# Optimization experiments

Measured on AMD Instinct MI355X. Metric: run time of the kernel, lower is better.

## Reference

```python
import jax, jax.numpy as jnp
import numpy as np

E = 1024  # embed_dim
H = 16    # num_heads
D = E // H  # head_dim


def setup_inputs() -> dict:
    key = jax.random.key(0)
    ks = jax.random.split(key, 9)
    s = 0.02
    return {
        "hidden_state": jax.random.normal(ks[0], (4, 1024, E), jnp.float32),
        "Wq": jax.random.normal(ks[1], (H, D, E), jnp.float32) * s,
        "bq": jax.random.normal(ks[2], (H, D), jnp.float32) * s,
        "Wk": jax.random.normal(ks[3], (H, D, E), jnp.float32) * s,
        "bk": jax.random.normal(ks[4], (H, D), jnp.float32) * s,
        "Wv": jax.random.normal(ks[5], (H, D, E), jnp.float32) * s,
        "bv": jax.random.normal(ks[6], (H, D), jnp.float32) * s,
        "Wo": jax.random.normal(ks[7], (E, E), jnp.float32) * s,
        "bo": jax.random.normal(ks[8], (E,), jnp.float32) * s,
    }


def _mha(x, Wq, bq, Wk, bk, Wv, bv, Wo, bo):
    # Per-head linear projections (torch Linear: y = x W^T + b), batched over heads.
    q = jnp.einsum("bse,hde->bhsd", x, Wq) + bq[None, :, None, :]
    k = jnp.einsum("bse,hde->bhsd", x, Wk) + bk[None, :, None, :]
    v = jnp.einsum("bse,hde->bhsd", x, Wv) + bv[None, :, None, :]
    scores = jnp.einsum("bhsd,bhtd->bhst", q, k) / jnp.sqrt(jnp.asarray(D, x.dtype))
    w = jax.nn.softmax(scores, axis=-1)  # F.softmax default -> last dim
    o = jnp.einsum("bhst,bhtd->bhsd", w, v)
    # concat heads along last dim: [B,S,H*D] in head order (matches torch.cat)
    B, _, S, _ = o.shape
    o = jnp.transpose(o, (0, 2, 1, 3)).reshape(B, S, H * D)
    return o @ Wo.T + bo


def reference(hidden_state, Wq, bq, Wk, bk, Wv, bv, Wo, bo):
    return _mha(hidden_state, Wq, bq, Wk, bk, Wv, bv, Wo, bo)
```

## Files before the change

kernel.cpp:

```cpp
#include <hip/hip_runtime.h>
#include <hip/hip_bf16.h>
#include <stdint.h>

#define E_DIM 1024
#define H_NUM 16
#define D_DIM 64
#define B_NUM 4
#define S_LEN 1024

typedef __attribute__((ext_vector_type(8))) short bf16x8;
typedef __attribute__((ext_vector_type(4))) short bf16x4;
typedef __attribute__((ext_vector_type(4))) float f32x4;

#define SOFTMAX_C2 0.18033688011112042f

__device__ inline ushort f2b(float x) {
    __hip_bfloat16 h = __float2bfloat16(x);
    return *(ushort*)&h;
}
__device__ inline uint pk2(float a, float b) {
    __hip_bfloat162 h = __float22bfloat162_rn(make_float2(a, b));
    return *(uint*)&h;
}

__device__ inline void gld16(const ushort* g, ushort* l) {
    __builtin_amdgcn_global_load_lds((const __attribute__((address_space(1))) void*)g,
                                     (__attribute__((address_space(3))) void*)l, 16, 0, 0);
}

__global__ __launch_bounds__(256)
void convert_all(const float* __restrict__ X,  const float* __restrict__ Wq,
                 const float* __restrict__ Wk, const float* __restrict__ Wv,
                 const float* __restrict__ Wo,
                 ushort* __restrict__ Xb, ushort* __restrict__ Wcat,
                 ushort* __restrict__ Wob)
{
    const int bid = blockIdx.x;
    const float* src; ushort* dst; size_t off;
    if (bid < 4096)      { src = X;  dst = Xb;   off = (size_t)bid * 1024; }
    else if (bid < 5120) { src = Wq; dst = Wcat;              off = (size_t)(bid - 4096) * 1024; }
    else if (bid < 6144) { src = Wk; dst = Wcat + (1u << 20); off = (size_t)(bid - 5120) * 1024; }
    else if (bid < 7168) { src = Wv; dst = Wcat + (2u << 20); off = (size_t)(bid - 6144) * 1024; }
    else                 { src = Wo; dst = Wob;               off = (size_t)(bid - 7168) * 1024; }
    const size_t i = off + (size_t)threadIdx.x * 4;
    float4 v = *(const float4*)&src[i];
    ushort4 o;
    o.x = f2b(v.x); o.y = f2b(v.y); o.z = f2b(v.z); o.w = f2b(v.w);
    *(ushort4*)&dst[i] = o;
}

template<int MODE>
__global__ __launch_bounds__(256)
void gemm128(const ushort* __restrict__ A, const ushort* __restrict__ Bw,
             const float* __restrict__ b0, const float* __restrict__ b1,
             const float* __restrict__ b2,
             ushort* __restrict__ Qb, ushort* __restrict__ Kb,
             ushort* __restrict__ Vt_g, float* __restrict__ Cout, int K)
{
    __shared__ __align__(16) ushort SM[12288];
    ushort* As = SM;
    ushort* Bs = SM + 8192;

    const int tid  = threadIdx.x;
    const int wave = tid >> 6;
    const int lane = tid & 63;
    const int quad = lane >> 4;
    const int l16  = lane & 15;
    const int wm   = wave & 1;
    const int wn   = wave >> 1;
    const int m0   = blockIdx.x * 128;
    const int n0   = blockIdx.y * 64;

    f32x4 acc[4][2] = {};

#pragma unroll
    for (int i = 0; i < 2; ++i) {
        const int e = i * 256 + tid;
        gld16(&A[(size_t)(m0 + (e >> 2)) * K + (e & 3) * 8], &As[e * 8]);
    }
    gld16(&Bw[(size_t)(n0 + (tid >> 2)) * K + (tid & 3) * 8], &Bs[tid * 8]);
    __syncthreads();

    const int nk = K >> 5;
    for (int ki = 0; ki < nk; ++ki) {
        const int cur = ki & 1;
        if (ki + 1 < nk) {
            const int k0 = (ki + 1) << 5;
#pragma unroll
            for (int i = 0; i < 2; ++i) {
                const int e = i * 256 + tid;
                gld16(&A[(size_t)(m0 + (e >> 2)) * K + k0 + (e & 3) * 8],
                      &As[(cur ^ 1) * 4096 + e * 8]);
            }
            gld16(&Bw[(size_t)(n0 + (tid >> 2)) * K + k0 + (tid & 3) * 8],
                  &Bs[(cur ^ 1) * 2048 + tid * 8]);
        }

        bf16x8 af[4], bf[2];
#pragma unroll
        for (int mi = 0; mi < 4; ++mi)
            af[mi] = *(const bf16x8*)&As[cur * 4096 + (wm * 64 + mi * 16 + l16) * 32 + quad * 8];
#pragma unroll
        for (int ni = 0; ni < 2; ++ni)
            bf[ni] = *(const bf16x8*)&Bs[cur * 2048 + (wn * 32 + ni * 16 + l16) * 32 + quad * 8];
#pragma unroll
        for (int mi = 0; mi < 4; ++mi)
#pragma unroll
            for (int ni = 0; ni < 2; ++ni)
                acc[mi][ni] = __builtin_amdgcn_mfma_f32_16x16x32_bf16(af[mi], bf[ni], acc[mi][ni], 0, 0, 0);
        __syncthreads();
    }

    if (MODE == 0) {
        const int seg   = n0 >> 10;
        const int cbase = n0 & 1023;
        const float* bp = (seg == 0) ? b0 : (seg == 1) ? b1 : b2;
        const float scl = (seg == 0) ? SOFTMAX_C2 : 1.0f;

        if (seg < 2) {
            ushort* T = SM;
#pragma unroll
            for (int ni = 0; ni < 2; ++ni) {
                const int nloc = wn * 32 + ni * 16 + l16;
                const float bv = bp[cbase + nloc];
#pragma unroll
                for (int mi = 0; mi < 4; ++mi)
#pragma unroll
                    for (int r = 0; r < 4; ++r)
                        T[(wm * 64 + mi * 16 + quad * 4 + r) * 72 + nloc] =
                            f2b((acc[mi][ni][r] + bv) * scl);
            }
            __syncthreads();
            ushort* dst = (seg == 0) ? Qb : Kb;
            const int row = tid >> 1, half = tid & 1;
            const ushort* s = &T[row * 72 + half * 32];
            ushort* d = &dst[(size_t)(m0 + row) * 1024 + cbase + half * 32];
#pragma unroll
            for (int j = 0; j < 4; ++j)
                *(uint4*)(d + j * 8) = *(const uint4*)(s + j * 8);
        } else {
            ushort* Tt = SM;
            const int hh = cbase >> 6;
            const int b  = m0 >> 10, sbase = m0 & 1023;
#pragma unroll
            for (int ni = 0; ni < 2; ++ni) {
                const int nloc = wn * 32 + ni * 16 + l16;
                const float bv = bp[cbase + nloc];
#pragma unroll
                for (int mi = 0; mi < 4; ++mi) {
                    const int mloc = wm * 64 + mi * 16 + quad * 4;
                    ushort4 pk;
                    pk.x = f2b(acc[mi][ni][0] + bv);
                    pk.y = f2b(acc[mi][ni][1] + bv);
                    pk.z = f2b(acc[mi][ni][2] + bv);
                    pk.w = f2b(acc[mi][ni][3] + bv);
                    *(ushort4*)&Tt[nloc * 136 + mloc] = pk;
                }
            }
            __syncthreads();
            const int nrow = tid >> 2, qtr = tid & 3;
            const ushort* s = &Tt[nrow * 136 + qtr * 32];
            ushort* d = &Vt_g[(((size_t)(b * 16 + hh)) * 64 + nrow) * 1024 + sbase + qtr * 32];
#pragma unroll
            for (int j = 0; j < 4; ++j)
                *(uint4*)(d + j * 8) = *(const uint4*)(s + j * 8);
        }
    } else {
        float* Tf = (float*)SM;
        float bv[2];
#pragma unroll
        for (int ni = 0; ni < 2; ++ni)
            bv[ni] = b0[n0 + wn * 32 + ni * 16 + l16];
#pragma unroll
        for (int p = 0; p < 2; ++p) {
            if (wm == p) {
#pragma unroll
                for (int ni = 0; ni < 2; ++ni) {
                    const int nloc = wn * 32 + ni * 16 + l16;
#pragma unroll
                    for (int mi = 0; mi < 4; ++mi)
#pragma unroll
                        for (int r = 0; r < 4; ++r)
                            Tf[(mi * 16 + quad * 4 + r) * 68 + nloc] = acc[mi][ni][r] + bv[ni];
                }
            }
            __syncthreads();
            const int row = tid >> 2, q4 = tid & 3;
            const float* s = &Tf[row * 68 + q4 * 16];
            float* d = &Cout[(size_t)(m0 + p * 64 + row) * 1024 + n0 + q4 * 16];
#pragma unroll
            for (int j = 0; j < 4; ++j)
                *(float4*)(d + j * 4) = *(const float4*)(s + j * 4);
            __syncthreads();
        }
    }
}

__global__ __launch_bounds__(256)
void attention5(const ushort* __restrict__ Qg, const ushort* __restrict__ Kg,
                const ushort* __restrict__ Vg, ushort* __restrict__ Og)
{
    __shared__ ushort S[4][64][68];

    const int tid  = threadIdx.x;
    const int w    = tid >> 6;
    const int lane = tid & 63;
    const int quad = lane >> 4;
    const int l16  = lane & 15;

    const int qt = blockIdx.x;
    const int bh = blockIdx.y;
    const int b  = bh >> 4;
    const int h  = bh & 15;
    const size_t tbase = ((size_t)b * S_LEN) * E_DIM + (size_t)h * D_DIM;
    const size_t vbase = (size_t)bh * D_DIM * S_LEN;

    const int sr = tid >> 3;
    const int c8 = (tid & 7) * 8;

#pragma unroll
    for (int g = 0; g < 4; ++g) {
        const int rr = sr + g * 32;
        *(uint4*)&S[2 + (rr >> 6)][rr & 63][c8] =
            *(const uint4*)&Qg[tbase + (size_t)(qt * 128 + rr) * E_DIM + c8];
    }
#pragma unroll
    for (int g = 0; g < 2; ++g) {
        const int rr = sr + g * 32;
        *(uint4*)&S[0][rr][c8] = *(const uint4*)&Kg[tbase + (size_t)rr * E_DIM + c8];
        *(uint4*)&S[1][rr][c8] = *(const uint4*)&Vg[vbase + (size_t)rr * S_LEN + c8];
    }
    __syncthreads();

    bf16x8 qf[2][2];
#pragma unroll
    for (int u = 0; u < 2; ++u) {
        qf[u][0] = *(const bf16x8*)&S[2 + u][w * 16 + l16][quad * 8];
        qf[u][1] = *(const bf16x8*)&S[2 + u][w * 16 + l16][32 + quad * 8];
    }
    __syncthreads();

    float lq[2] = {0.0f, 0.0f};
    f32x4 oacc[2][4] = {};

    for (int kt = 0; kt < 16; ++kt) {
        const int cur = kt & 1;

        uint4 kpre[2], vpre[2];
        if (kt < 15) {
#pragma unroll
            for (int g = 0; g < 2; ++g) {
                const int rr = sr + g * 32;
                kpre[g] = *(const uint4*)&Kg[tbase + (size_t)((kt + 1) * 64 + rr) * E_DIM + c8];
                vpre[g] = *(const uint4*)&Vg[vbase + (size_t)rr * S_LEN + (kt + 1) * 64 + c8];
            }
        }

        f32x4 sacc[2][4] = {};
#pragma unroll
        for (int mt = 0; mt < 4; ++mt)
#pragma unroll
            for (int ks = 0; ks < 2; ++ks) {
                bf16x8 kf = *(const bf16x8*)&S[cur * 2][mt * 16 + l16][ks * 32 + quad * 8];
                sacc[0][mt] = __builtin_amdgcn_mfma_f32_16x16x32_bf16(kf, qf[0][ks], sacc[0][mt], 0, 0, 0);
                sacc[1][mt] = __builtin_amdgcn_mfma_f32_16x16x32_bf16(kf, qf[1][ks], sacc[1][mt], 0, 0, 0);
            }

        bf16x4 pf[2][4];
#pragma unroll
        for (int u = 0; u < 2; ++u) {
            float rs = 0.0f;
#pragma unroll
            for (int mt = 0; mt < 4; ++mt) {
                float p0 = exp2f(sacc[u][mt][0]);
                float p1 = exp2f(sacc[u][mt][1]);
                float p2 = exp2f(sacc[u][mt][2]);
                float p3 = exp2f(sacc[u][mt][3]);
                rs += (p0 + p1) + (p2 + p3);
                union { uint uu[2]; bf16x4 v; } pk;
                pk.uu[0] = pk2(p0, p1);
                pk.uu[1] = pk2(p2, p3);
                pf[u][mt] = pk.v;
            }
            lq[u] += rs;
        }

#pragma unroll
        for (int nb = 0; nb < 4; ++nb)
#pragma unroll
            for (int kb = 0; kb < 4; ++kb) {
                bf16x4 vf = *(const bf16x4*)&S[cur * 2 + 1][nb * 16 + l16][kb * 16 + quad * 4];
                oacc[0][nb] = __builtin_amdgcn_mfma_f32_16x16x16bf16_1k(pf[0][kb], vf, oacc[0][nb], 0, 0, 0);
                oacc[1][nb] = __builtin_amdgcn_mfma_f32_16x16x16bf16_1k(pf[1][kb], vf, oacc[1][nb], 0, 0, 0);
            }

        if (kt < 15) {
            const int nxt = cur ^ 1;
#pragma unroll
            for (int g = 0; g < 2; ++g) {
                const int rr = sr + g * 32;
                *(uint4*)&S[nxt * 2][rr][c8]     = kpre[g];
                *(uint4*)&S[nxt * 2 + 1][rr][c8] = vpre[g];
            }
        }
        __syncthreads();
    }

#pragma unroll
    for (int u = 0; u < 2; ++u) {
        float l = lq[u];
        l += __shfl_xor(l, 16);
        l += __shfl_xor(l, 32);
        const float linv = 1.0f / l;
        float lC[4];
#pragma unroll
        for (int r = 0; r < 4; ++r) lC[r] = __shfl(linv, quad * 4 + r);
#pragma unroll
        for (int nb = 0; nb < 4; ++nb)
#pragma unroll
            for (int r = 0; r < 4; ++r) {
                const int q = qt * 128 + u * 64 + w * 16 + quad * 4 + r;
                const int d = nb * 16 + l16;
                Og[tbase + (size_t)q * E_DIM + d] = f2b(oacc[u][nb][r] * lC[r]);
            }
    }
}

extern "C" void kernel_launch(void* const* d_in, const int* in_sizes, int n_in,
                              void* d_out, int out_size, void* d_ws, size_t ws_size,
                              hipStream_t stream)
{
    (void)in_sizes; (void)n_in; (void)out_size; (void)ws_size;

    const float* X  = (const float*)d_in[0];
    const float* Wq = (const float*)d_in[1];
    const float* bq = (const float*)d_in[2];
    const float* Wk = (const float*)d_in[3];
    const float* bk = (const float*)d_in[4];
    const float* Wv = (const float*)d_in[5];
    const float* bv = (const float*)d_in[6];
    const float* Wo = (const float*)d_in[7];
    const float* bo = (const float*)d_in[8];

    const size_t MEG = 1u << 20;
    ushort* ws   = (ushort*)d_ws;
    ushort* Xb   = ws;
    ushort* Wcat = ws + 4 * MEG;
    ushort* Wob  = ws + 7 * MEG;
    ushort* Qb   = ws + 8 * MEG;
    ushort* Kb   = ws + 12 * MEG;
    ushort* Vtg  = ws + 16 * MEG;
    ushort* AO   = Xb;

    dim3 blk(256);

    convert_all<<<8192, blk, 0, stream>>>(X, Wq, Wk, Wv, Wo, Xb, Wcat, Wob);

    gemm128<0><<<dim3(32, 48), blk, 0, stream>>>(Xb, Wcat, bq, bk, bv,
                                                 Qb, Kb, Vtg, nullptr, E_DIM);

    attention5<<<dim3(8, 64), blk, 0, stream>>>(Qb, Kb, Vtg, AO);

    gemm128<1><<<dim3(32, 16), blk, 0, stream>>>(AO, Wob, bo, nullptr, nullptr,
                                                 nullptr, nullptr, nullptr,
                                                 (float*)d_out, E_DIM);
}
```

Measured before the change: 208.1 us.

## Split attention over key halves with combine kernel and smaller output-GEMM tiles

Attention is now split along the key dimension into two halves (grid z=2) with 64-query tiles and 32-key steps. Each half writes unnormalised bf16 partial outputs and row sums, which a new combine kernel adds and normalises into the head-concatenated buffer. The output projection becomes a dedicated 64x64-tile GEMM to launch more blocks. This raises block count and occupancy on the many-CU GPU, at the cost of an extra kernel launch, extra partial-result traffic, and rounding partials to bf16 before summing.

```diff
diff --git a/kernel.cpp b/kernel.cpp
--- a/kernel.cpp
+++ b/kernel.cpp
@@ -17,6 +17,10 @@
 __device__ inline ushort f2b(float x) {
     __hip_bfloat16 h = __float2bfloat16(x);
     return *(ushort*)&h;
+}
+__device__ inline float b2f(ushort u) {
+    __hip_bfloat16 h = *(__hip_bfloat16*)&u;
+    return __bfloat162float(h);
 }
 __device__ inline uint pk2(float a, float b) {
     __hip_bfloat162 h = __float22bfloat162_rn(make_float2(a, b));
@@ -49,13 +53,12 @@
     *(ushort4*)&dst[i] = o;
 }
 
-template<int MODE>
 __global__ __launch_bounds__(256)
-void gemm128(const ushort* __restrict__ A, const ushort* __restrict__ Bw,
-             const float* __restrict__ b0, const float* __restrict__ b1,
-             const float* __restrict__ b2,
-             ushort* __restrict__ Qb, ushort* __restrict__ Kb,
-             ushort* __restrict__ Vt_g, float* __restrict__ Cout, int K)
+void gemm_qkv(const ushort* __restrict__ A, const ushort* __restrict__ Bw,
+              const float* __restrict__ b0, const float* __restrict__ b1,
+              const float* __restrict__ b2,
+              ushort* __restrict__ Qb, ushort* __restrict__ Kb,
+              ushort* __restrict__ Vt_g, int K)
 {
     __shared__ __align__(16) ushort SM[12288];
     ushort* As = SM;
@@ -111,96 +114,68 @@
         __syncthreads();
     }
 
-    if (MODE == 0) {
-        const int seg   = n0 >> 10;
-        const int cbase = n0 & 1023;
-        const float* bp = (seg == 0) ? b0 : (seg == 1) ? b1 : b2;
-        const float scl = (seg == 0) ? SOFTMAX_C2 : 1.0f;
-
-        if (seg < 2) {
-            ushort* T = SM;
-#pragma unroll
-            for (int ni = 0; ni < 2; ++ni) {
-                const int nloc = wn * 32 + ni * 16 + l16;
-                const float bv = bp[cbase + nloc];
-#pragma unroll
-                for (int mi = 0; mi < 4; ++mi)
-#pragma unroll
-                    for (int r = 0; r < 4; ++r)
-                        T[(wm * 64 + mi * 16 + quad * 4 + r) * 72 + nloc] =
-                            f2b((acc[mi][ni][r] + bv) * scl);
+    const int seg   = n0 >> 10;
+    const int cbase = n0 & 1023;
+    const float* bp = (seg == 0) ? b0 : (seg == 1) ? b1 : b2;
+    const float scl = (seg == 0) ? SOFTMAX_C2 : 1.0f;
+
+    if (seg < 2) {
+        ushort* T = SM;
+#pragma unroll
+        for (int ni = 0; ni < 2; ++ni) {
+            const int nloc = wn * 32 + ni * 16 + l16;
+            const float bv = bp[cbase + nloc];
+#pragma unroll
+            for (int mi = 0; mi < 4; ++mi)
+#pragma unroll
+                for (int r = 0; r < 4; ++r)
+                    T[(wm * 64 + mi * 16 + quad * 4 + r) * 72 + nloc] =
+                        f2b((acc[mi][ni][r] + bv) * scl);
+        }
+        __syncthreads();
+        ushort* dst = (seg == 0) ? Qb : Kb;
+        const int row = tid >> 1, half = tid & 1;
+        const ushort* s = &T[row * 72 + half * 32];
+        ushort* d = &dst[(size_t)(m0 + row) * 1024 + cbase + half * 32];
+#pragma unroll
+        for (int j = 0; j < 4; ++j)
+            *(uint4*)(d + j * 8) = *(const uint4*)(s + j * 8);
+    } else {
+        ushort* Tt = SM;
+        const int hh = cbase >> 6;
+        const int b  = m0 >> 10, sbase = m0 & 1023;
+#pragma unroll
+        for (int ni = 0; ni < 2; ++ni) {
+            const int nloc = wn * 32 + ni * 16 + l16;
+            const float bv = bp[cbase + nloc];
+#pragma unroll
+            for (int mi = 0; mi < 4; ++mi) {
+                const int mloc = wm * 64 + mi * 16 + quad * 4;
+                ushort4 pk;
+                pk.x = f2b(acc[mi][ni][0] + bv);
+                pk.y = f2b(acc[mi][ni][1] + bv);
+                pk.z = f2b(acc[mi][ni][2] + bv);
+                pk.w = f2b(acc[mi][ni][3] + bv);
+                *(ushort4*)&Tt[nloc * 136 + mloc] = pk;
             }
-            __syncthreads();
-            ushort* dst = (seg == 0) ? Qb : Kb;
-            const int row = tid >> 1, half = tid & 1;
-            const ushort* s = &T[row * 72 + half * 32];
-            ushort* d = &dst[(size_t)(m0 + row) * 1024 + cbase + half * 32];
-#pragma unroll
-            for (int j = 0; j < 4; ++j)
-                *(uint4*)(d + j * 8) = *(const uint4*)(s + j * 8);
-        } else {
-            ushort* Tt = SM;
-            const int hh = cbase >> 6;
-            const int b  = m0 >> 10, sbase = m0 & 1023;
-#pragma unroll
-            for (int ni = 0; ni < 2; ++ni) {
-                const int nloc = wn * 32 + ni * 16 + l16;
-                const float bv = bp[cbase + nloc];
-#pragma unroll
-                for (int mi = 0; mi < 4; ++mi) {
-                    const int mloc = wm * 64 + mi * 16 + quad * 4;
-                    ushort4 pk;
-                    pk.x = f2b(acc[mi][ni][0] + bv);
-                    pk.y = f2b(acc[mi][ni][1] + bv);
-                    pk.z = f2b(acc[mi][ni][2] + bv);
-                    pk.w = f2b(acc[mi][ni][3] + bv);
-                    *(ushort4*)&Tt[nloc * 136 + mloc] = pk;
-                }
-            }
-            __syncthreads();
-            const int nrow = tid >> 2, qtr = tid & 3;
-            const ushort* s = &Tt[nrow * 136 + qtr * 32];
-            ushort* d = &Vt_g[(((size_t)(b * 16 + hh)) * 64 + nrow) * 1024 + sbase + qtr * 32];
-#pragma unroll
-            for (int j = 0; j < 4; ++j)
-                *(uint4*)(d + j * 8) = *(const uint4*)(s + j * 8);
-        }
-    } else {
-        float* Tf = (float*)SM;
-        float bv[2];
-#pragma unroll
-        for (int ni = 0; ni < 2; ++ni)
-            bv[ni] = b0[n0 + wn * 32 + ni * 16 + l16];
-#pragma unroll
-        for (int p = 0; p < 2; ++p) {
-            if (wm == p) {
-#pragma unroll
-                for (int ni = 0; ni < 2; ++ni) {
-                    const int nloc = wn * 32 + ni * 16 + l16;
-#pragma unroll
-                    for (int mi = 0; mi < 4; ++mi)
-#pragma unroll
-                        for (int r = 0; r < 4; ++r)
-                            Tf[(mi * 16 + quad * 4 + r) * 68 + nloc] = acc[mi][ni][r] + bv[ni];
-                }
-            }
-            __syncthreads();
-            const int row = tid >> 2, q4 = tid & 3;
-            const float* s = &Tf[row * 68 + q4 * 16];
-            float* d = &Cout[(size_t)(m0 + p * 64 + row) * 1024 + n0 + q4 * 16];
-#pragma unroll
-            for (int j = 0; j < 4; ++j)
-                *(float4*)(d + j * 4) = *(const float4*)(s + j * 4);
-            __syncthreads();
-        }
+        }
+        __syncthreads();
+        const int nrow = tid >> 2, qtr = tid & 3;
+        const ushort* s = &Tt[nrow * 136 + qtr * 32];
+        ushort* d = &Vt_g[(((size_t)(b * 16 + hh)) * 64 + nrow) * 1024 + sbase + qtr * 32];
+#pragma unroll
+        for (int j = 0; j < 4; ++j)
+            *(uint4*)(d + j * 8) = *(const uint4*)(s + j * 8);
     }
 }
 
 __global__ __launch_bounds__(256)
-void attention5(const ushort* __restrict__ Qg, const ushort* __restrict__ Kg,
-                const ushort* __restrict__ Vg, ushort* __restrict__ Og)
-{
-    __shared__ ushort S[4][64][68];
+void attention6(const ushort* __restrict__ Qg, const ushort* __restrict__ Kg,
+                const ushort* __restrict__ Vg,
+                ushort* __restrict__ Opart, float* __restrict__ Lpart)
+{
+    __shared__ ushort Kb[2][32][72];
+    __shared__ ushort Vb[2][64][40];
 
     const int tid  = threadIdx.x;
     const int w    = tid >> 6;
@@ -210,119 +185,187 @@
 
     const int qt = blockIdx.x;
     const int bh = blockIdx.y;
+    const int th = blockIdx.z;
     const int b  = bh >> 4;
     const int h  = bh & 15;
     const size_t tbase = ((size_t)b * S_LEN) * E_DIM + (size_t)h * D_DIM;
     const size_t vbase = (size_t)bh * D_DIM * S_LEN;
-
-    const int sr = tid >> 3;
-    const int c8 = (tid & 7) * 8;
-
-#pragma unroll
-    for (int g = 0; g < 4; ++g) {
-        const int rr = sr + g * 32;
-        *(uint4*)&S[2 + (rr >> 6)][rr & 63][c8] =
-            *(const uint4*)&Qg[tbase + (size_t)(qt * 128 + rr) * E_DIM + c8];
-    }
-#pragma unroll
-    for (int g = 0; g < 2; ++g) {
-        const int rr = sr + g * 32;
-        *(uint4*)&S[0][rr][c8] = *(const uint4*)&Kg[tbase + (size_t)rr * E_DIM + c8];
-        *(uint4*)&S[1][rr][c8] = *(const uint4*)&Vg[vbase + (size_t)rr * S_LEN + c8];
+    const int t0 = th * 512;
+
+    const ushort* qrow = Qg + tbase + (size_t)(qt * 64 + w * 16 + l16) * E_DIM + quad * 8;
+    bf16x8 qf[2];
+    qf[0] = *(const bf16x8*)qrow;
+    qf[1] = *(const bf16x8*)(qrow + 32);
+
+    {
+        const int kr = tid >> 3, kc = (tid & 7) * 8;
+        *(uint4*)&Kb[0][kr][kc] = *(const uint4*)&Kg[tbase + (size_t)(t0 + kr) * E_DIM + kc];
+        const int vr = tid >> 2, vc = (tid & 3) * 8;
+        *(uint4*)&Vb[0][vr][vc] = *(const uint4*)&Vg[vbase + (size_t)vr * S_LEN + t0 + vc];
     }
     __syncthreads();
 
-    bf16x8 qf[2][2];
-#pragma unroll
-    for (int u = 0; u < 2; ++u) {
-        qf[u][0] = *(const bf16x8*)&S[2 + u][w * 16 + l16][quad * 8];
-        qf[u][1] = *(const bf16x8*)&S[2 + u][w * 16 + l16][32 + quad * 8];
-    }
-    __syncthreads();
-
-    float lq[2] = {0.0f, 0.0f};
-    f32x4 oacc[2][4] = {};
+    float lq = 0.0f;
+    f32x4 oacc[4] = {};
 
     for (int kt = 0; kt < 16; ++kt) {
         const int cur = kt & 1;
 
-        uint4 kpre[2], vpre[2];
+        uint4 kpre, vpre;
+        const int kr = tid >> 3, kc = (tid & 7) * 8;
+        const int vr = tid >> 2, vc = (tid & 3) * 8;
         if (kt < 15) {
-#pragma unroll
-            for (int g = 0; g < 2; ++g) {
-                const int rr = sr + g * 32;
-                kpre[g] = *(const uint4*)&Kg[tbase + (size_t)((kt + 1) * 64 + rr) * E_DIM + c8];
-                vpre[g] = *(const uint4*)&Vg[vbase + (size_t)rr * S_LEN + (kt + 1) * 64 + c8];
+            const int tg = t0 + (kt + 1) * 32;
+            kpre = *(const uint4*)&Kg[tbase + (size_t)(tg + kr) * E_DIM + kc];
+            vpre = *(const uint4*)&Vg[vbase + (size_t)vr * S_LEN + tg + vc];
+        }
+
+        f32x4 sacc[2] = {};
+#pragma unroll
+        for (int mt = 0; mt < 2; ++mt)
+#pragma unroll
+            for (int ks = 0; ks < 2; ++ks) {
+                bf16x8 kf = *(const bf16x8*)&Kb[cur][mt * 16 + l16][ks * 32 + quad * 8];
+                sacc[mt] = __builtin_amdgcn_mfma_f32_16x16x32_bf16(kf, qf[ks], sacc[mt], 0, 0, 0);
             }
-        }
-
-        f32x4 sacc[2][4] = {};
-#pragma unroll
-        for (int mt = 0; mt < 4; ++mt)
-#pragma unroll
-            for (int ks = 0; ks < 2; ++ks) {
-                bf16x8 kf = *(const bf16x8*)&S[cur * 2][mt * 16 + l16][ks * 32 + quad * 8];
-                sacc[0][mt] = __builtin_amdgcn_mfma_f32_16x16x32_bf16(kf, qf[0][ks], sacc[0][mt], 0, 0, 0);
-                sacc[1][mt] = __builtin_amdgcn_mfma_f32_16x16x32_bf16(kf, qf[1][ks], sacc[1][mt], 0, 0, 0);
-            }
-
-        bf16x4 pf[2][4];
-#pragma unroll
-        for (int u = 0; u < 2; ++u) {
-            float rs = 0.0f;
-#pragma unroll
-            for (int mt = 0; mt < 4; ++mt) {
-                float p0 = exp2f(sacc[u][mt][0]);
-                float p1 = exp2f(sacc[u][mt][1]);
-                float p2 = exp2f(sacc[u][mt][2]);
-                float p3 = exp2f(sacc[u][mt][3]);
-                rs += (p0 + p1) + (p2 + p3);
-                union { uint uu[2]; bf16x4 v; } pk;
-                pk.uu[0] = pk2(p0, p1);
-                pk.uu[1] = pk2(p2, p3);
-                pf[u][mt] = pk.v;
-            }
-            lq[u] += rs;
-        }
+
+        bf16x4 pf[2];
+        float rs = 0.0f;
+#pragma unroll
+        for (int mt = 0; mt < 2; ++mt) {
+            float p0 = exp2f(sacc[mt][0]);
+            float p1 = exp2f(sacc[mt][1]);
+            float p2 = exp2f(sacc[mt][2]);
+            float p3 = exp2f(sacc[mt][3]);
+            rs += (p0 + p1) + (p2 + p3);
+            union { uint uu[2]; bf16x4 v; } pk;
+            pk.uu[0] = pk2(p0, p1);
+            pk.uu[1] = pk2(p2, p3);
+            pf[mt] = pk.v;
+        }
+        lq += rs;
 
 #pragma unroll
         for (int nb = 0; nb < 4; ++nb)
 #pragma unroll
-            for (int kb = 0; kb < 4; ++kb) {
-                bf16x4 vf = *(const bf16x4*)&S[cur * 2 + 1][nb * 16 + l16][kb * 16 + quad * 4];
-                oacc[0][nb] = __builtin_amdgcn_mfma_f32_16x16x16bf16_1k(pf[0][kb], vf, oacc[0][nb], 0, 0, 0);
-                oacc[1][nb] = __builtin_amdgcn_mfma_f32_16x16x16bf16_1k(pf[1][kb], vf, oacc[1][nb], 0, 0, 0);
+            for (int kb = 0; kb < 2; ++kb) {
+                bf16x4 vf = *(const bf16x4*)&Vb[cur][nb * 16 + l16][kb * 16 + quad * 4];
+                oacc[nb] = __builtin_amdgcn_mfma_f32_16x16x16bf16_1k(pf[kb], vf, oacc[nb], 0, 0, 0);
             }
 
         if (kt < 15) {
             const int nxt = cur ^ 1;
-#pragma unroll
-            for (int g = 0; g < 2; ++g) {
-                const int rr = sr + g * 32;
-                *(uint4*)&S[nxt * 2][rr][c8]     = kpre[g];
-                *(uint4*)&S[nxt * 2 + 1][rr][c8] = vpre[g];
-            }
+            *(uint4*)&Kb[nxt][kr][kc] = kpre;
+            *(uint4*)&Vb[nxt][vr][vc] = vpre;
         }
         __syncthreads();
     }
 
-#pragma unroll
-    for (int u = 0; u < 2; ++u) {
-        float l = lq[u];
-        l += __shfl_xor(l, 16);
-        l += __shfl_xor(l, 32);
-        const float linv = 1.0f / l;
-        float lC[4];
-#pragma unroll
-        for (int r = 0; r < 4; ++r) lC[r] = __shfl(linv, quad * 4 + r);
-#pragma unroll
-        for (int nb = 0; nb < 4; ++nb)
-#pragma unroll
-            for (int r = 0; r < 4; ++r) {
-                const int q = qt * 128 + u * 64 + w * 16 + quad * 4 + r;
-                const int d = nb * 16 + l16;
-                Og[tbase + (size_t)q * E_DIM + d] = f2b(oacc[u][nb][r] * lC[r]);
-            }
+    lq += __shfl_xor(lq, 16);
+    lq += __shfl_xor(lq, 32);
+    const size_t obase = ((size_t)(th * 64 + bh)) * S_LEN;
+    if (lane < 16)
+        Lpart[obase + qt * 64 + w * 16 + l16] = lq;
+
+    ushort* T = &Kb[0][0][0];
+#pragma unroll
+    for (int nb = 0; nb < 4; ++nb)
+#pragma unroll
+        for (int r = 0; r < 4; ++r)
+            T[(w * 16 + quad * 4 + r) * 72 + nb * 16 + l16] = f2b(oacc[nb][r]);
+    __syncthreads();
+    {
+        const int row = tid >> 2, c16 = (tid & 3) * 16;
+        const ushort* s = &T[row * 72 + c16];
+        ushort* d = &Opart[(obase + qt * 64 + row) * 64 + c16];
+        *(uint4*)(d)     = *(const uint4*)(s);
+        *(uint4*)(d + 8) = *(const uint4*)(s + 8);
+    }
+}
+
+__global__ __launch_bounds__(256)
+void combine(const ushort* __restrict__ Opart, const float* __restrict__ Lpart,
+             ushort* __restrict__ AO)
+{
+    const int bh = blockIdx.x >> 6;
+    const int qc = blockIdx.x & 63;
+    const int b  = bh >> 4;
+    const int h  = bh & 15;
+    const int q  = qc * 16 + (threadIdx.x >> 4);
+    const int d4 = (threadIdx.x & 15) * 4;
+
+    const size_t i0 = (((size_t)bh) * S_LEN + q) * 64 + d4;
+    const size_t i1 = (((size_t)(64 + bh)) * S_LEN + q) * 64 + d4;
+    ushort4 o0 = *(const ushort4*)&Opart[i0];
+    ushort4 o1 = *(const ushort4*)&Opart[i1];
+    const float l0 = Lpart[(size_t)bh * S_LEN + q];
+    const float l1 = Lpart[(size_t)(64 + bh) * S_LEN + q];
+    const float li = 1.0f / (l0 + l1);
+
+    union { uint uu[2]; ushort4 v; } r;
+    r.uu[0] = pk2((b2f(o0.x) + b2f(o1.x)) * li, (b2f(o0.y) + b2f(o1.y)) * li);
+    r.uu[1] = pk2((b2f(o0.z) + b2f(o1.z)) * li, (b2f(o0.w) + b2f(o1.w)) * li);
+    AO[((size_t)(b * S_LEN + q)) * E_DIM + h * 64 + d4] = r.v.x;
+    *(ushort4*)&AO[((size_t)(b * S_LEN + q)) * E_DIM + h * 64 + d4] = r.v;
+}
+
+__global__ __launch_bounds__(256)
+void gemm_out(const ushort* __restrict__ A, const ushort* __restrict__ Bw,
+              const float* __restrict__ bias, float* __restrict__ Cout, int K)
+{
+    __shared__ __align__(16) ushort SM[8704];
+    ushort* As = SM;
+    ushort* Bs = SM + 4096;
+
+    const int tid  = threadIdx.x;
+    const int w    = tid >> 6;
+    const int lane = tid & 63;
+    const int quad = lane >> 4;
+    const int l16  = lane & 15;
+    const int m0   = blockIdx.x * 64;
+    const int n0   = blockIdx.y * 64;
+
+    f32x4 acc[4] = {};
+
+    gld16(&A[(size_t)(m0 + (tid >> 2)) * K + (tid & 3) * 8], &As[tid * 8]);
+    gld16(&Bw[(size_t)(n0 + (tid >> 2)) * K + (tid & 3) * 8], &Bs[tid * 8]);
+    __syncthreads();
+
+    const int nk = K >> 5;
+    for (int ki = 0; ki < nk; ++ki) {
+        const int cur = ki & 1;
+        if (ki + 1 < nk) {
+            const int k0 = (ki + 1) << 5;
+            gld16(&A[(size_t)(m0 + (tid >> 2)) * K + k0 + (tid & 3) * 8],
+                  &As[(cur ^ 1) * 2048 + tid * 8]);
+            gld16(&Bw[(size_t)(n0 + (tid >> 2)) * K + k0 + (tid & 3) * 8],
+                  &Bs[(cur ^ 1) * 2048 + tid * 8]);
+        }
+        bf16x8 af = *(const bf16x8*)&As[cur * 2048 + (w * 16 + l16) * 32 + quad * 8];
+#pragma unroll
+        for (int nb = 0; nb < 4; ++nb) {
+            bf16x8 bf = *(const bf16x8*)&Bs[cur * 2048 + (nb * 16 + l16) * 32 + quad * 8];
+            acc[nb] = __builtin_amdgcn_mfma_f32_16x16x32_bf16(af, bf, acc[nb], 0, 0, 0);
+        }
+        __syncthreads();
+    }
+
+    float* Tf = (float*)SM;
+#pragma unroll
+    for (int nb = 0; nb < 4; ++nb) {
+        const float bv = bias[n0 + nb * 16 + l16];
+#pragma unroll
+        for (int r = 0; r < 4; ++r)
+            Tf[(w * 16 + quad * 4 + r) * 68 + nb * 16 + l16] = acc[nb][r] + bv;
+    }
+    __syncthreads();
+    {
+        const int row = tid >> 2, c16 = (tid & 3) * 16;
+        const float* s = &Tf[row * 68 + c16];
+        float* d = &Cout[(size_t)(m0 + row) * 1024 + n0 + c16];
+#pragma unroll
+        for (int j = 0; j < 4; ++j)
+            *(float4*)(d + j * 4) = *(const float4*)(s + j * 4);
     }
 }
 
@@ -343,25 +386,27 @@
     const float* bo = (const float*)d_in[8];
 
     const size_t MEG = 1u << 20;
-    ushort* ws   = (ushort*)d_ws;
-    ushort* Xb   = ws;
-    ushort* Wcat = ws + 4 * MEG;
-    ushort* Wob  = ws + 7 * MEG;
-    ushort* Qb   = ws + 8 * MEG;
-    ushort* Kb   = ws + 12 * MEG;
-    ushort* Vtg  = ws + 16 * MEG;
-    ushort* AO   = Xb;
+    ushort* ws    = (ushort*)d_ws;
+    ushort* Xb    = ws;
+    ushort* Wcat  = ws + 4 * MEG;
+    ushort* Wob   = ws + 7 * MEG;
+    ushort* Qb    = ws + 8 * MEG;
+    ushort* Kb    = ws + 12 * MEG;
+    ushort* Vtg   = ws + 16 * MEG;
+    ushort* Opart = ws + 20 * MEG;
+    float*  Lpart = (float*)(ws + 28 * MEG);
+    ushort* AO    = Xb;
 
     dim3 blk(256);
 
     convert_all<<<8192, blk, 0, stream>>>(X, Wq, Wk, Wv, Wo, Xb, Wcat, Wob);
 
-    gemm128<0><<<dim3(32, 48), blk, 0, stream>>>(Xb, Wcat, bq, bk, bv,
-                                                 Qb, Kb, Vtg, nullptr, E_DIM);
-
-    attention5<<<dim3(8, 64), blk, 0, stream>>>(Qb, Kb, Vtg, AO);
-
-    gemm128<1><<<dim3(32, 16), blk, 0, stream>>>(AO, Wob, bo, nullptr, nullptr,
-                                                 nullptr, nullptr, nullptr,
-                                                 (float*)d_out, E_DIM);
-}
+    gemm_qkv<<<dim3(32, 48), blk, 0, stream>>>(Xb, Wcat, bq, bk, bv,
+                                               Qb, Kb, Vtg, E_DIM);
+
+    attention6<<<dim3(16, 64, 2), blk, 0, stream>>>(Qb, Kb, Vtg, Opart, Lpart);
+
+    combine<<<4096, blk, 0, stream>>>(Opart, Lpart, AO);
+
+    gemm_out<<<dim3(64, 16), blk, 0, stream>>>(AO, Wob, bo, (float*)d_out, E_DIM);
+}
```

Result: faster. 203.3 us (-2.3%).
